# Kernel optimization log

Measured on AMD Instinct MI355X. Metric: run time of the kernel, lower is better.

Reference implementation:

```python
import jax, jax.numpy as jnp
import numpy as np

B, NPG, K, DIN, DOUT, EMB, HEADS = 64, 1024, 32, 512, 512, 32, 4
HD = EMB // HEADS  # head dim = 8


def layernorm(x, g, b, eps=1e-5):
    m = jnp.mean(x, axis=-1, keepdims=True)
    v = jnp.var(x, axis=-1, keepdims=True)
    return (x - m) / jnp.sqrt(v + eps) * g + b


def _xavier(key, out_f, in_f, gain=0.5):
    std = gain * np.sqrt(2.0 / (in_f + out_f))
    return jax.random.normal(key, (out_f, in_f), dtype=jnp.float32) * std


def setup_inputs() -> dict:
    key = jax.random.key(0)
    ks = jax.random.split(key, 16)
    N = B * NPG
    x = jax.random.normal(ks[0], (N, DIN), dtype=jnp.float32)
    # roughly orthonormal-column scale for eigenvectors
    eigenvectors = jax.random.normal(ks[1], (N, K), dtype=jnp.float32) / np.sqrt(NPG)
    eigenvalues = jax.random.uniform(ks[2], (B * K,), dtype=jnp.float32) * 2.0
    eig_mask = jnp.ones((B * K,), dtype=bool)
    batch = jnp.repeat(jnp.arange(B, dtype=jnp.int64), NPG)
    z = jnp.zeros
    o = jnp.ones
    return {
        "x": x, "eigenvectors": eigenvectors, "eigenvalues": eigenvalues,
        "eig_mask": eig_mask, "batch": batch,
        "W1": _xavier(ks[3], 32, 1), "b1": z(32), "g1": o(32), "be1": z(32),
        "W2": _xavier(ks[4], 32, 32), "b2": z(32), "g2": o(32), "be2": z(32),
        "Wqkv": _xavier(ks[5], 3 * EMB, EMB), "bqkv": z(3 * EMB),
        "Wo": _xavier(ks[6], EMB, EMB), "bo": z(EMB),
        "Wf1": _xavier(ks[7], 64, 32), "bf1": z(64),
        "Wf2": _xavier(ks[8], 1, 64), "bf2": z(1),
        "Wp": _xavier(ks[9], DOUT, DIN), "bp": z(DOUT),
        "gp": o(DOUT), "bep": z(DOUT),
    }


def reference(x, eigenvectors, eigenvalues, eig_mask, batch,
              W1, b1, g1, be1, W2, b2, g2, be2,
              Wqkv, bqkv, Wo, bo, Wf1, bf1, Wf2, bf2, Wp, bp, gp, bep):
    # ---- eigenvalue set encoder (batched over all graphs at once) ----
    ev = eigenvalues.reshape(B, K, 1)                       # [B,K,1]
    h = ev @ W1.T + b1                                      # [B,K,32]
    h = jax.nn.relu(layernorm(h, g1, be1))
    h = layernorm(h @ W2.T + b2, g2, be2)                   # [B,K,32]
    # ---- multi-head self-attention over the K eigenvalues ----
    padding = ~eig_mask.reshape(B, K)                       # True = masked out
    qkv = h @ Wqkv.T + bqkv                                 # [B,K,96]
    q, k_, v = jnp.split(qkv, 3, axis=-1)
    def heads(t):
        return t.reshape(B, K, HEADS, HD).transpose(0, 2, 1, 3)  # [B,H,K,hd]
    q, k_, v = heads(q), heads(k_), heads(v)
    scores = jnp.einsum('bhqd,bhkd->bhqk', q, k_) / np.sqrt(HD)
    scores = jnp.where(padding[:, None, None, :], -1e9, scores)
    attn = jax.nn.softmax(scores, axis=-1)
    ctx = jnp.einsum('bhqk,bhkd->bhqd', attn, v)
    ctx = ctx.transpose(0, 2, 1, 3).reshape(B, K, EMB)
    ctx = ctx @ Wo.T + bo                                   # [B,K,32]
    # ---- filter generator ----
    f = jnp.tanh(jax.nn.relu(ctx @ Wf1.T + bf1) @ Wf2.T + bf2)[..., 0]  # [B,K]
    filters = jnp.where(padding, 0.0, f)
    # ---- spectral filtering per graph (equal-size graphs -> reshape) ----
    xg = x.reshape(B, NPG, DIN)
    vg = eigenvectors.reshape(B, NPG, K)
    x_freq = jnp.einsum('bnk,bnd->bkd', vg, xg)             # U^T x
    x_spat = jnp.einsum('bnk,bkd->bnd', vg, filters[:, :, None] * x_freq)
    out = layernorm(x_spat @ Wp.T + bp, gp, bep)            # [B,NPG,DOUT]
    return out.reshape(B * NPG, DOUT)
```

## Files before the change

### kernel.cpp

```cpp
#include <hip/hip_runtime.h>
#include <math.h>

#define B    64
#define NPG  1024
#define KEIG 32
#define DIN  512
#define DOUT 512
#define NPART 8

typedef float f32x4 __attribute__((ext_vector_type(4)));

__device__ __forceinline__ float rsum32(float v) {
    v += __shfl_xor(v, 1, 32);
    v += __shfl_xor(v, 2, 32);
    v += __shfl_xor(v, 4, 32);
    v += __shfl_xor(v, 8, 32);
    v += __shfl_xor(v, 16, 32);
    return v;
}
__device__ __forceinline__ float rmax32(float v) {
    v = fmaxf(v, __shfl_xor(v, 1, 32));
    v = fmaxf(v, __shfl_xor(v, 2, 32));
    v = fmaxf(v, __shfl_xor(v, 4, 32));
    v = fmaxf(v, __shfl_xor(v, 8, 32));
    v = fmaxf(v, __shfl_xor(v, 16, 32));
    return v;
}
__device__ __forceinline__ float rsum64(float v) {
    v += __shfl_xor(v, 1, 64);
    v += __shfl_xor(v, 2, 64);
    v += __shfl_xor(v, 4, 64);
    v += __shfl_xor(v, 8, 64);
    v += __shfl_xor(v, 16, 64);
    v += __shfl_xor(v, 32, 64);
    return v;
}

__global__ __launch_bounds__(1024) void k1_filters(
    const float* __restrict__ eigenvalues,
    const float* __restrict__ W1,  const float* __restrict__ b1,
    const float* __restrict__ g1,  const float* __restrict__ be1,
    const float* __restrict__ W2,  const float* __restrict__ b2,
    const float* __restrict__ g2,  const float* __restrict__ be2,
    const float* __restrict__ Wqkv,const float* __restrict__ bqkv,
    const float* __restrict__ Wo,  const float* __restrict__ bo,
    const float* __restrict__ Wf1, const float* __restrict__ bf1,
    const float* __restrict__ Wf2, const float* __restrict__ bf2,
    float* __restrict__ filters)
{
    __shared__ float wts[224][33];
    __shared__ float hA[KEIG][33];
    __shared__ float hB[KEIG][33];
    __shared__ float qkv[KEIG][97];
    __shared__ float attn[4 * 1064];

    const int t = threadIdx.x;
    const int k = t >> 5;
    const int j = t & 31;
    const int b = blockIdx.x;

    {
        const int row = t >> 5, i = t & 31;
        wts[row][i]       = W2[t];
        wts[32 + row][i]  = Wqkv[t];
        wts[64 + row][i]  = Wqkv[1024 + t];
        wts[96 + row][i]  = Wqkv[2048 + t];
        wts[128 + row][i] = Wo[t];
        wts[160 + row][i] = Wf1[t];
        wts[192 + row][i] = Wf1[1024 + t];
    }

    const float ev = eigenvalues[b * KEIG + k];
    float h1 = ev * W1[j] + b1[j];
    {
        float m = rsum32(h1) * (1.f / 32.f);
        float d = h1 - m;
        float q = rsum32(d * d);
        float r = rsqrtf(q * (1.f / 32.f) + 1e-5f);
        h1 = fmaxf(d * r * g1[j] + be1[j], 0.f);
    }
    hA[k][j] = h1;
    __syncthreads();

    {
        float a = b2[j];
        #pragma unroll
        for (int i = 0; i < 32; ++i) a += hA[k][i] * wts[j][i];
        float m = rsum32(a) * (1.f / 32.f);
        float d = a - m;
        float q = rsum32(d * d);
        float r = rsqrtf(q * (1.f / 32.f) + 1e-5f);
        hB[k][j] = d * r * g2[j] + be2[j];
    }
    __syncthreads();

    {
        float aq = bqkv[j], ak = bqkv[32 + j], av = bqkv[64 + j];
        #pragma unroll
        for (int i = 0; i < 32; ++i) {
            float hv = hB[k][i];
            aq += hv * wts[32 + j][i];
            ak += hv * wts[64 + j][i];
            av += hv * wts[96 + j][i];
        }
        qkv[k][j]      = aq;
        qkv[k][32 + j] = ak;
        qkv[k][64 + j] = av;
    }
    __syncthreads();

    {
        const float inv = 0.35355339059327373f;
        float sc[4];
        #pragma unroll
        for (int hh = 0; hh < 4; ++hh) {
            float s = 0.f;
            #pragma unroll
            for (int d2 = 0; d2 < 8; ++d2)
                s += qkv[k][hh * 8 + d2] * qkv[j][32 + hh * 8 + d2];
            sc[hh] = s * inv;
        }
        #pragma unroll
        for (int hh = 0; hh < 4; ++hh) {
            float mx  = rmax32(sc[hh]);
            float e   = __expf(sc[hh] - mx);
            float den = rsum32(e);
            attn[hh * 1064 + k * 33 + j] = e / den;
        }
    }
    __syncthreads();

    {
        const int hh = j >> 3;
        float c = 0.f;
        #pragma unroll
        for (int k2 = 0; k2 < 32; ++k2)
            c += attn[hh * 1064 + k * 33 + k2] * qkv[k2][64 + j];
        hA[k][j] = c;
    }
    __syncthreads();

    {
        float o = bo[j];
        #pragma unroll
        for (int i = 0; i < 32; ++i) o += hA[k][i] * wts[128 + j][i];
        hB[k][j] = o;
    }
    __syncthreads();

    {
        float r0 = bf1[j], r1 = bf1[32 + j];
        #pragma unroll
        for (int i = 0; i < 32; ++i) {
            float ov = hB[k][i];
            r0 += ov * wts[160 + j][i];
            r1 += ov * wts[192 + j][i];
        }
        float fp = fmaxf(r0, 0.f) * Wf2[j] + fmaxf(r1, 0.f) * Wf2[32 + j];
        fp = rsum32(fp);
        if (j == 0) filters[b * KEIG + k] = tanhf(fp + bf2[0]);
    }
}

__global__ __launch_bounds__(256) void k2_xfreq_partial(
    const float* __restrict__ x, const float* __restrict__ eigvec,
    float* __restrict__ xfp)
{
    __shared__ float vtile[128][32];
    const int t  = threadIdx.x;
    const int b  = blockIdx.x >> 4;
    const int nc = (blockIdx.x >> 1) & 7;
    const int dh = blockIdx.x & 1;
    const int kq = t >> 6;
    const int ds = t & 63;
    const int d  = dh * 256 + ds * 4;
    const int n0 = nc * 128;

    const float* vb = eigvec + ((size_t)(b * NPG + n0)) * KEIG;
    #pragma unroll
    for (int e = 0; e < 16; ++e) {
        int idx = t + e * 256;
        ((float*)vtile)[idx] = vb[idx];
    }
    __syncthreads();

    float4 acc[8];
    #pragma unroll
    for (int i = 0; i < 8; ++i) acc[i] = make_float4(0.f, 0.f, 0.f, 0.f);

    const float* xb = x + ((size_t)(b * NPG + n0)) * DIN + d;
    #pragma unroll 4
    for (int n = 0; n < 128; ++n) {
        float4 xv = *(const float4*)(xb + (size_t)n * DIN);
        const float4* vp = (const float4*)&vtile[n][kq * 8];
        float4 v0 = vp[0], v1 = vp[1];
        acc[0].x += v0.x * xv.x; acc[0].y += v0.x * xv.y; acc[0].z += v0.x * xv.z; acc[0].w += v0.x * xv.w;
        acc[1].x += v0.y * xv.x; acc[1].y += v0.y * xv.y; acc[1].z += v0.y * xv.z; acc[1].w += v0.y * xv.w;
        acc[2].x += v0.z * xv.x; acc[2].y += v0.z * xv.y; acc[2].z += v0.z * xv.z; acc[2].w += v0.z * xv.w;
        acc[3].x += v0.w * xv.x; acc[3].y += v0.w * xv.y; acc[3].z += v0.w * xv.z; acc[3].w += v0.w * xv.w;
        acc[4].x += v1.x * xv.x; acc[4].y += v1.x * xv.y; acc[4].z += v1.x * xv.z; acc[4].w += v1.x * xv.w;
        acc[5].x += v1.y * xv.x; acc[5].y += v1.y * xv.y; acc[5].z += v1.y * xv.z; acc[5].w += v1.y * xv.w;
        acc[6].x += v1.z * xv.x; acc[6].y += v1.z * xv.y; acc[6].z += v1.z * xv.z; acc[6].w += v1.z * xv.w;
        acc[7].x += v1.w * xv.x; acc[7].y += v1.w * xv.y; acc[7].z += v1.w * xv.z; acc[7].w += v1.w * xv.w;
    }

    #pragma unroll
    for (int kk = 0; kk < 8; ++kk) {
        int kg = kq * 8 + kk;
        *(float4*)(xfp + (((size_t)nc * B + b) * KEIG + kg) * DIN + d) = acc[kk];
    }
}

__global__ __launch_bounds__(256) void k2b_combine(
    const float* __restrict__ xfp, const float* __restrict__ filters,
    float* __restrict__ F)
{
    const int t = threadIdx.x;
    const int m = blockIdx.x * 2 + (t >> 7);
    const int dp = (t & 127) * 4;

    const float* base = xfp + (size_t)m * DIN + dp;
    float4 s = *(const float4*)base;
    #pragma unroll
    for (int q = 1; q < NPART; ++q) {
        float4 sq = *(const float4*)(base + (size_t)q * (B * KEIG * DIN));
        s.x += sq.x; s.y += sq.y; s.z += sq.z; s.w += sq.w;
    }
    const float f = filters[m];
    float4 o = make_float4(s.x * f, s.y * f, s.z * f, s.w * f);
    *(float4*)(F + (size_t)m * DIN + dp) = o;
}

__global__ __launch_bounds__(256) void k3_G(
    const float* __restrict__ F, const float* __restrict__ Wp,
    float* __restrict__ G)
{
    __shared__ float a_lds[64][65];
    __shared__ float b_lds[64][65];

    const int t   = threadIdx.x;
    const int mt  = blockIdx.x >> 3;
    const int ot  = blockIdx.x & 7;
    const int m0  = mt * 64;
    const int o0  = ot * 64;
    const int tr  = t >> 4;
    const int tc  = t & 15;
    const int col4 = tc * 4;

    float acc[4][4] = {{0.f}};

    for (int d0 = 0; d0 < DIN; d0 += 64) {
        __syncthreads();
        #pragma unroll
        for (int p = 0; p < 4; ++p) {
            int r = p * 16 + tr;
            float4 s = *(const float4*)(F + (size_t)(m0 + r) * DIN + d0 + col4);
            a_lds[r][col4 + 0] = s.x;
            a_lds[r][col4 + 1] = s.y;
            a_lds[r][col4 + 2] = s.z;
            a_lds[r][col4 + 3] = s.w;
        }
        #pragma unroll
        for (int p = 0; p < 4; ++p) {
            int r = p * 16 + tr;
            float4 w = *(const float4*)(Wp + (size_t)(o0 + r) * DIN + d0 + col4);
            b_lds[r][col4 + 0] = w.x;
            b_lds[r][col4 + 1] = w.y;
            b_lds[r][col4 + 2] = w.z;
            b_lds[r][col4 + 3] = w.w;
        }
        __syncthreads();
        #pragma unroll 4
        for (int dd = 0; dd < 64; ++dd) {
            float a0 = a_lds[tr * 4 + 0][dd];
            float a1 = a_lds[tr * 4 + 1][dd];
            float a2 = a_lds[tr * 4 + 2][dd];
            float a3 = a_lds[tr * 4 + 3][dd];
            float b0 = b_lds[tc * 4 + 0][dd];
            float b1 = b_lds[tc * 4 + 1][dd];
            float b2 = b_lds[tc * 4 + 2][dd];
            float b3 = b_lds[tc * 4 + 3][dd];
            acc[0][0] += a0 * b0; acc[0][1] += a0 * b1; acc[0][2] += a0 * b2; acc[0][3] += a0 * b3;
            acc[1][0] += a1 * b0; acc[1][1] += a1 * b1; acc[1][2] += a1 * b2; acc[1][3] += a1 * b3;
            acc[2][0] += a2 * b0; acc[2][1] += a2 * b1; acc[2][2] += a2 * b2; acc[2][3] += a2 * b3;
            acc[3][0] += a3 * b0; acc[3][1] += a3 * b1; acc[3][2] += a3 * b2; acc[3][3] += a3 * b3;
        }
    }
    #pragma unroll
    for (int i = 0; i < 4; ++i) {
        float4 v = make_float4(acc[i][0], acc[i][1], acc[i][2], acc[i][3]);
        *(float4*)(G + (size_t)(m0 + tr * 4 + i) * DOUT + o0 + col4) = v;
    }
}

__global__ __launch_bounds__(256, 2) void k4_out(
    const float* __restrict__ eigvec, const float* __restrict__ G,
    const float* __restrict__ bp, const float* __restrict__ gp,
    const float* __restrict__ bep, float* __restrict__ out)
{
    __shared__ float gsh[KEIG][DOUT];
    __shared__ float vgt[KEIG][68];

    const int t  = threadIdx.x;
    const int b  = blockIdx.x >> 4;
    const int n0 = (blockIdx.x & 15) * 64;

    const float4* G4 = (const float4*)(G + (size_t)b * KEIG * DOUT);
    float4* gsh4 = (float4*)gsh;
    #pragma unroll
    for (int e = 0; e < 16; ++e)
        gsh4[t + e * 256] = G4[t + e * 256];

    const float* vb = eigvec + ((size_t)(b * NPG + n0)) * KEIG;
    #pragma unroll
    for (int e = 0; e < 8; ++e) {
        int idx = t + e * 256;
        vgt[idx & 31][idx >> 5] = vb[idx];
    }
    __syncthreads();

    const int w  = t >> 6;
    const int l  = t & 63;
    const int c0 = 4 * l;

    const float4 bpA = *(const float4*)(bp + c0);
    const float4 bpB = *(const float4*)(bp + 256 + c0);
    const float4 gpA = *(const float4*)(gp + c0);
    const float4 gpB = *(const float4*)(gp + 256 + c0);
    const float4 beA = *(const float4*)(bep + c0);
    const float4 beB = *(const float4*)(bep + 256 + c0);

    for (int gq = 0; gq < 4; ++gq) {
        const int rbase = w * 16 + gq * 4;
        float4 aA[4], aB[4];
        #pragma unroll
        for (int r = 0; r < 4; ++r) { aA[r] = bpA; aB[r] = bpB; }

        #pragma unroll 8
        for (int k = 0; k < KEIG; ++k) {
            const float4 ga = *(const float4*)&gsh[k][c0];
            const float4 gb = *(const float4*)&gsh[k][256 + c0];
            const float4 vv = *(const float4*)&vgt[k][rbase];
            const float vr[4] = {vv.x, vv.y, vv.z, vv.w};
            #pragma unroll
            for (int r = 0; r < 4; ++r) {
                aA[r].x += vr[r] * ga.x; aA[r].y += vr[r] * ga.y;
                aA[r].z += vr[r] * ga.z; aA[r].w += vr[r] * ga.w;
                aB[r].x += vr[r] * gb.x; aB[r].y += vr[r] * gb.y;
                aB[r].z += vr[r] * gb.z; aB[r].w += vr[r] * gb.w;
            }
        }

        #pragma unroll
        for (int r = 0; r < 4; ++r) {
            float s = aA[r].x + aA[r].y + aA[r].z + aA[r].w
                    + aB[r].x + aB[r].y + aB[r].z + aB[r].w;
            float q = aA[r].x * aA[r].x + aA[r].y * aA[r].y
                    + aA[r].z * aA[r].z + aA[r].w * aA[r].w
                    + aB[r].x * aB[r].x + aB[r].y * aB[r].y
                    + aB[r].z * aB[r].z + aB[r].w * aB[r].w;
            s = rsum64(s);
            q = rsum64(q);
            float m    = s * (1.f / 512.f);
            float rstd = rsqrtf(q * (1.f / 512.f) - m * m + 1e-5f);

            float4 oA, oB;
            oA.x = (aA[r].x - m) * rstd * gpA.x + beA.x;
            oA.y = (aA[r].y - m) * rstd * gpA.y + beA.y;
            oA.z = (aA[r].z - m) * rstd * gpA.z + beA.z;
            oA.w = (aA[r].w - m) * rstd * gpA.w + beA.w;
            oB.x = (aB[r].x - m) * rstd * gpB.x + beB.x;
            oB.y = (aB[r].y - m) * rstd * gpB.y + beB.y;
            oB.z = (aB[r].z - m) * rstd * gpB.z + beB.z;
            oB.w = (aB[r].w - m) * rstd * gpB.w + beB.w;

            size_t row = (size_t)b * NPG + n0 + rbase + r;
            *(float4*)(out + row * DOUT + c0)       = oA;
            *(float4*)(out + row * DOUT + 256 + c0) = oB;
        }
    }
}

extern "C" void kernel_launch(void* const* d_in, const int* in_sizes, int n_in,
                              void* d_out, int out_size, void* d_ws, size_t ws_size,
                              hipStream_t stream) {
    (void)in_sizes; (void)n_in; (void)out_size; (void)ws_size;
    const float* x    = (const float*)d_in[0];
    const float* vg   = (const float*)d_in[1];
    const float* ev   = (const float*)d_in[2];
    const float* W1   = (const float*)d_in[5];
    const float* b1   = (const float*)d_in[6];
    const float* g1   = (const float*)d_in[7];
    const float* be1  = (const float*)d_in[8];
    const float* W2   = (const float*)d_in[9];
    const float* b2   = (const float*)d_in[10];
    const float* g2   = (const float*)d_in[11];
    const float* be2  = (const float*)d_in[12];
    const float* Wqkv = (const float*)d_in[13];
    const float* bqkv = (const float*)d_in[14];
    const float* Wo   = (const float*)d_in[15];
    const float* bo   = (const float*)d_in[16];
    const float* Wf1  = (const float*)d_in[17];
    const float* bf1  = (const float*)d_in[18];
    const float* Wf2  = (const float*)d_in[19];
    const float* bf2  = (const float*)d_in[20];
    const float* Wp   = (const float*)d_in[21];
    const float* bp   = (const float*)d_in[22];
    const float* gp   = (const float*)d_in[23];
    const float* bep  = (const float*)d_in[24];

    float* outf    = (float*)d_out;
    float* ws      = (float*)d_ws;
    float* filters = ws;
    float* G       = ws + 4096;
    float* xfp     = outf;
    float* F       = outf + 16777216;

    hipLaunchKernelGGL(k1_filters, dim3(B), dim3(1024), 0, stream,
                       ev, W1, b1, g1, be1, W2, b2, g2, be2,
                       Wqkv, bqkv, Wo, bo, Wf1, bf1, Wf2, bf2, filters);
    hipLaunchKernelGGL(k2_xfreq_partial, dim3(B * 16), dim3(256), 0, stream,
                       x, vg, xfp);
    hipLaunchKernelGGL(k2b_combine, dim3(1024), dim3(256), 0, stream,
                       xfp, filters, F);
    hipLaunchKernelGGL(k3_G, dim3(32 * 8), dim3(256), 0, stream,
                       F, Wp, G);
    hipLaunchKernelGGL(k4_out, dim3(B * 16), dim3(256), 0, stream,
                       vg, G, bp, gp, bep, outf);
}
```

Before: 144.0 us.

## Use bf16 MFMA for the final eigvec-times-G product with transposed bf16 G

After: 131.7 us. 8.5% less time.

```diff
diff --git a/kernel.cpp b/kernel.cpp
--- a/kernel.cpp
+++ b/kernel.cpp
@@ -8,7 +8,14 @@
 #define DOUT 512
 #define NPART 8
 
-typedef float f32x4 __attribute__((ext_vector_type(4)));
+typedef float  f32x4  __attribute__((ext_vector_type(4)));
+typedef short  bf16x8 __attribute__((ext_vector_type(8)));
+
+__device__ __forceinline__ unsigned short f2bf(float x) {
+    union { float f; unsigned int u; } v; v.f = x;
+    unsigned int r = v.u + 0x7FFFu + ((v.u >> 16) & 1u);
+    return (unsigned short)(r >> 16);
+}
 
 __device__ __forceinline__ float rsum32(float v) {
     v += __shfl_xor(v, 1, 32);
@@ -24,15 +31,6 @@
     v = fmaxf(v, __shfl_xor(v, 4, 32));
     v = fmaxf(v, __shfl_xor(v, 8, 32));
     v = fmaxf(v, __shfl_xor(v, 16, 32));
-    return v;
-}
-__device__ __forceinline__ float rsum64(float v) {
-    v += __shfl_xor(v, 1, 64);
-    v += __shfl_xor(v, 2, 64);
-    v += __shfl_xor(v, 4, 64);
-    v += __shfl_xor(v, 8, 64);
-    v += __shfl_xor(v, 16, 64);
-    v += __shfl_xor(v, 32, 64);
     return v;
 }
 
@@ -233,7 +231,7 @@
 
 __global__ __launch_bounds__(256) void k3_G(
     const float* __restrict__ F, const float* __restrict__ Wp,
-    float* __restrict__ G)
+    unsigned short* __restrict__ Gt)
 {
     __shared__ float a_lds[64][65];
     __shared__ float b_lds[64][65];
@@ -288,95 +286,109 @@
     }
     #pragma unroll
     for (int i = 0; i < 4; ++i) {
-        float4 v = make_float4(acc[i][0], acc[i][1], acc[i][2], acc[i][3]);
-        *(float4*)(G + (size_t)(m0 + tr * 4 + i) * DOUT + o0 + col4) = v;
-    }
-}
-
-__global__ __launch_bounds__(256, 2) void k4_out(
-    const float* __restrict__ eigvec, const float* __restrict__ G,
+        int m  = m0 + tr * 4 + i;
+        int bb = m >> 5, kk = m & 31;
+        #pragma unroll
+        for (int j = 0; j < 4; ++j) {
+            int o = o0 + tc * 4 + j;
+            Gt[((size_t)bb * DOUT + o) * KEIG + kk] = f2bf(acc[i][j]);
+        }
+    }
+}
+
+__global__ __launch_bounds__(256, 1) void k4_out(
+    const float* __restrict__ eigvec, const unsigned short* __restrict__ Gt,
     const float* __restrict__ bp, const float* __restrict__ gp,
     const float* __restrict__ bep, float* __restrict__ out)
 {
-    __shared__ float gsh[KEIG][DOUT];
-    __shared__ float vgt[KEIG][68];
+    __shared__ unsigned short gt_lds[512][40];
+    __shared__ float prm[3 * 512];
 
     const int t  = threadIdx.x;
     const int b  = blockIdx.x >> 4;
     const int n0 = (blockIdx.x & 15) * 64;
 
-    const float4* G4 = (const float4*)(G + (size_t)b * KEIG * DOUT);
-    float4* gsh4 = (float4*)gsh;
-    #pragma unroll
-    for (int e = 0; e < 16; ++e)
-        gsh4[t + e * 256] = G4[t + e * 256];
-
-    const float* vb = eigvec + ((size_t)(b * NPG + n0)) * KEIG;
-    #pragma unroll
-    for (int e = 0; e < 8; ++e) {
+    {
+        const unsigned short* src = Gt + (size_t)b * (DOUT * KEIG);
+        #pragma unroll
+        for (int e = 0; e < 8; ++e) {
+            int c = t + e * 256;
+            int row = c >> 2, part = c & 3;
+            bf16x8 v = *(const bf16x8*)(src + c * 8);
+            *(bf16x8*)&gt_lds[row][part * 8] = v;
+        }
+    }
+    #pragma unroll
+    for (int e = 0; e < 6; ++e) {
         int idx = t + e * 256;
-        vgt[idx & 31][idx >> 5] = vb[idx];
+        prm[idx] = (idx < 512) ? bp[idx]
+                 : (idx < 1024) ? gp[idx - 512] : bep[idx - 1024];
     }
     __syncthreads();
 
     const int w  = t >> 6;
     const int l  = t & 63;
-    const int c0 = 4 * l;
-
-    const float4 bpA = *(const float4*)(bp + c0);
-    const float4 bpB = *(const float4*)(bp + 256 + c0);
-    const float4 gpA = *(const float4*)(gp + c0);
-    const float4 gpB = *(const float4*)(gp + 256 + c0);
-    const float4 beA = *(const float4*)(bep + c0);
-    const float4 beB = *(const float4*)(bep + 256 + c0);
-
-    for (int gq = 0; gq < 4; ++gq) {
-        const int rbase = w * 16 + gq * 4;
-        float4 aA[4], aB[4];
-        #pragma unroll
-        for (int r = 0; r < 4; ++r) { aA[r] = bpA; aB[r] = bpB; }
-
-        #pragma unroll 8
-        for (int k = 0; k < KEIG; ++k) {
-            const float4 ga = *(const float4*)&gsh[k][c0];
-            const float4 gb = *(const float4*)&gsh[k][256 + c0];
-            const float4 vv = *(const float4*)&vgt[k][rbase];
-            const float vr[4] = {vv.x, vv.y, vv.z, vv.w};
-            #pragma unroll
-            for (int r = 0; r < 4; ++r) {
-                aA[r].x += vr[r] * ga.x; aA[r].y += vr[r] * ga.y;
-                aA[r].z += vr[r] * ga.z; aA[r].w += vr[r] * ga.w;
-                aB[r].x += vr[r] * gb.x; aB[r].y += vr[r] * gb.y;
-                aB[r].z += vr[r] * gb.z; aB[r].w += vr[r] * gb.w;
-            }
-        }
-
-        #pragma unroll
-        for (int r = 0; r < 4; ++r) {
-            float s = aA[r].x + aA[r].y + aA[r].z + aA[r].w
-                    + aB[r].x + aB[r].y + aB[r].z + aB[r].w;
-            float q = aA[r].x * aA[r].x + aA[r].y * aA[r].y
-                    + aA[r].z * aA[r].z + aA[r].w * aA[r].w
-                    + aB[r].x * aB[r].x + aB[r].y * aB[r].y
-                    + aB[r].z * aB[r].z + aB[r].w * aB[r].w;
-            s = rsum64(s);
-            q = rsum64(q);
-            float m    = s * (1.f / 512.f);
-            float rstd = rsqrtf(q * (1.f / 512.f) - m * m + 1e-5f);
-
-            float4 oA, oB;
-            oA.x = (aA[r].x - m) * rstd * gpA.x + beA.x;
-            oA.y = (aA[r].y - m) * rstd * gpA.y + beA.y;
-            oA.z = (aA[r].z - m) * rstd * gpA.z + beA.z;
-            oA.w = (aA[r].w - m) * rstd * gpA.w + beA.w;
-            oB.x = (aB[r].x - m) * rstd * gpB.x + beB.x;
-            oB.y = (aB[r].y - m) * rstd * gpB.y + beB.y;
-            oB.z = (aB[r].z - m) * rstd * gpB.z + beB.z;
-            oB.w = (aB[r].w - m) * rstd * gpB.w + beB.w;
-
-            size_t row = (size_t)b * NPG + n0 + rbase + r;
-            *(float4*)(out + row * DOUT + c0)       = oA;
-            *(float4*)(out + row * DOUT + 256 + c0) = oB;
+    const int cl = l & 15;
+    const int g  = l >> 4;
+    const int kb = g * 8;
+
+    bf16x8 afrag;
+    {
+        const float* ar = eigvec + ((size_t)(b * NPG + n0 + w * 16 + cl)) * KEIG + kb;
+        float4 a0 = *(const float4*)(ar);
+        float4 a1 = *(const float4*)(ar + 4);
+        afrag[0] = (short)f2bf(a0.x); afrag[1] = (short)f2bf(a0.y);
+        afrag[2] = (short)f2bf(a0.z); afrag[3] = (short)f2bf(a0.w);
+        afrag[4] = (short)f2bf(a1.x); afrag[5] = (short)f2bf(a1.y);
+        afrag[6] = (short)f2bf(a1.z); afrag[7] = (short)f2bf(a1.w);
+    }
+
+    f32x4 acc[32];
+    #pragma unroll
+    for (int ct = 0; ct < 32; ++ct) acc[ct] = (f32x4){0.f, 0.f, 0.f, 0.f};
+
+    #pragma unroll
+    for (int ct = 0; ct < 32; ++ct) {
+        bf16x8 bfrag = *(const bf16x8*)&gt_lds[ct * 16 + cl][kb];
+        acc[ct] = __builtin_amdgcn_mfma_f32_16x16x32_bf16(afrag, bfrag, acc[ct], 0, 0, 0);
+    }
+
+    float s[4] = {0.f, 0.f, 0.f, 0.f}, q[4] = {0.f, 0.f, 0.f, 0.f};
+    #pragma unroll
+    for (int ct = 0; ct < 32; ++ct) {
+        float bpc = prm[ct * 16 + cl];
+        #pragma unroll
+        for (int j = 0; j < 4; ++j) {
+            float v = acc[ct][j] + bpc;
+            s[j] += v; q[j] += v * v;
+        }
+    }
+    #pragma unroll
+    for (int off = 1; off < 16; off <<= 1) {
+        #pragma unroll
+        for (int j = 0; j < 4; ++j) {
+            s[j] += __shfl_xor(s[j], off, 16);
+            q[j] += __shfl_xor(q[j], off, 16);
+        }
+    }
+    float mh[4], rs[4];
+    #pragma unroll
+    for (int j = 0; j < 4; ++j) {
+        mh[j] = s[j] * (1.f / 512.f);
+        rs[j] = rsqrtf(q[j] * (1.f / 512.f) - mh[j] * mh[j] + 1e-5f);
+    }
+
+    const size_t rowbase = (size_t)b * NPG + n0 + w * 16 + g * 4;
+    #pragma unroll
+    for (int ct = 0; ct < 32; ++ct) {
+        int col = ct * 16 + cl;
+        float bpc = prm[col];
+        float gpc = prm[512 + col];
+        float bec = prm[1024 + col];
+        #pragma unroll
+        for (int j = 0; j < 4; ++j) {
+            float v = (acc[ct][j] + bpc - mh[j]) * rs[j] * gpc + bec;
+            __builtin_nontemporal_store(v, out + (rowbase + j) * DOUT + col);
         }
     }
 }
@@ -412,7 +424,7 @@
     float* outf    = (float*)d_out;
     float* ws      = (float*)d_ws;
     float* filters = ws;
-    float* G       = ws + 4096;
+    unsigned short* Gt = (unsigned short*)(ws + 4096);
     float* xfp     = outf;
     float* F       = outf + 16777216;
 
@@ -424,7 +436,7 @@
     hipLaunchKernelGGL(k2b_combine, dim3(1024), dim3(256), 0, stream,
                        xfp, filters, F);
     hipLaunchKernelGGL(k3_G, dim3(32 * 8), dim3(256), 0, stream,
-                       F, Wp, G);
+                       F, Wp, Gt);
     hipLaunchKernelGGL(k4_out, dim3(B * 16), dim3(256), 0, stream,
-                       vg, G, bp, gp, bep, outf);
-}
+                       vg, Gt, bp, gp, bep, outf);
+}
```
